# Kernel tuning notes

Measured on AMD Instinct MI355X. Metric: run time of the kernel, lower is better.

## Reference

```python
import jax, jax.numpy as jnp
import numpy as np

NUM_NODES = 512
HEADS = 4
IN_F = 256
OUT_F = 128
EPS = 1e-5


def _layernorm(x, g, b):
    mu = jnp.mean(x, axis=-1, keepdims=True)
    var = jnp.mean(jnp.square(x - mu), axis=-1, keepdims=True)
    return (x - mu) * jax.lax.rsqrt(var + EPS) * g + b


def setup_inputs() -> dict:
    key = jax.random.key(0)
    ks = jax.random.split(key, 16)
    N = 32 * NUM_NODES
    E = 262144
    s = 0.05
    return {
        "x": jax.random.normal(ks[0], (N, IN_F), jnp.float32),
        "edge_index": jax.random.randint(ks[1], (2, E), 0, N, jnp.int64),
        "W_l": jax.random.normal(ks[2], (IN_F, HEADS * OUT_F), jnp.float32) * s,
        "W_r": jax.random.normal(ks[3], (IN_F, HEADS * OUT_F), jnp.float32) * s,
        "att": jax.random.normal(ks[4], (HEADS, OUT_F), jnp.float32) * s,
        "gat_bias": jnp.zeros((OUT_F,), jnp.float32),
        "gat_gamma": jnp.ones((OUT_F,), jnp.float32),
        "gat_beta": jnp.zeros((OUT_F,), jnp.float32),
        "cnn_W": jax.random.normal(ks[5], (IN_F, OUT_F), jnp.float32) * s,
        "cnn_b": jnp.zeros((OUT_F,), jnp.float32),
        "conv_W": jax.random.normal(ks[6], (OUT_F, OUT_F, 7), jnp.float32) * s,
        "conv_b": jnp.zeros((OUT_F,), jnp.float32),
        "cnn_gamma": jnp.ones((OUT_F,), jnp.float32),
        "cnn_beta": jnp.zeros((OUT_F,), jnp.float32),
        "res_W": jax.random.normal(ks[7], (IN_F, OUT_F), jnp.float32) * s,
        "res_b": jnp.zeros((OUT_F,), jnp.float32),
        "fuse_gamma": jnp.ones((OUT_F,), jnp.float32),
        "fuse_beta": jnp.zeros((OUT_F,), jnp.float32),
    }


def reference(x, edge_index, W_l, W_r, att, gat_bias, gat_gamma, gat_beta,
              cnn_W, cnn_b, conv_W, conv_b, cnn_gamma, cnn_beta,
              res_W, res_b, fuse_gamma, fuse_beta):
    N = x.shape[0]
    B = N // NUM_NODES
    # --- GATv2 branch (add self-loops like PyG default) ---
    loop = jnp.arange(N, dtype=edge_index.dtype)
    src = jnp.concatenate([edge_index[0], loop])
    dst = jnp.concatenate([edge_index[1], loop])
    x_l = (x @ W_l).reshape(N, HEADS, OUT_F)
    x_r = (x @ W_r).reshape(N, HEADS, OUT_F)
    e = x_l[src] + x_r[dst]                      # [E+N, H, F]
    e = jnp.where(e > 0, e, 0.2 * e)             # leaky_relu, slope 0.2
    score = jnp.einsum('ehf,hf->eh', e, att)     # [E+N, H]
    m = jax.ops.segment_max(score, dst, num_segments=N)
    ex = jnp.exp(score - m[dst])
    denom = jax.ops.segment_sum(ex, dst, num_segments=N)
    alpha = ex / denom[dst]
    agg = jax.ops.segment_sum(alpha[:, :, None] * x_l[src], dst, num_segments=N)
    h_gat = jnp.mean(agg, axis=1) + gat_bias     # concat=False -> head mean
    h_gat = jnp.where(h_gat > 0, h_gat, 0.01 * h_gat)  # nn.LeakyReLU default
    h_gat = _layernorm(h_gat, gat_gamma, gat_beta)
    # --- CNN branch ---
    xc = x @ cnn_W + cnn_b                       # [N, F]
    xc = xc.reshape(B, NUM_NODES, OUT_F).transpose(0, 2, 1)  # [B, F, L]
    hc = jax.lax.conv_general_dilated(xc, conv_W, window_strides=(1,),
                                      padding=[(3, 3)],
                                      dimension_numbers=('NCW', 'OIW', 'NCW'))
    hc = hc + conv_b[None, :, None]
    hc = hc.transpose(0, 2, 1).reshape(N, OUT_F)
    hc = jax.nn.relu(hc)
    hc = _layernorm(hc, cnn_gamma, cnn_beta)
    # --- fuse + residual ---
    h = h_gat + hc + (x @ res_W + res_b)
    return _layernorm(h, fuse_gamma, fuse_beta)
```

## Files before the change

### kernel.cpp

```cpp
#include <hip/hip_runtime.h>
#include <hip/hip_bf16.h>
#include <math.h>

#define IN_F 256
#define OUT_F 128
#define HEADS 4
#define HF 512
#define NCAT 1280

typedef __hip_bfloat16 bf16;
typedef unsigned short ushort_t;
typedef unsigned char uchar_t;

using bf16x8 = __attribute__((ext_vector_type(8))) short;
using f32x4  = __attribute__((ext_vector_type(4))) float;

__device__ __forceinline__ float bflo(unsigned u) { return __uint_as_float(u << 16); }
__device__ __forceinline__ float bfhi(unsigned u) { return __uint_as_float(u & 0xffff0000u); }
__device__ __forceinline__ float bf2f(ushort_t u) { return __uint_as_float((unsigned)u << 16); }
__device__ __forceinline__ ushort_t f2bf(float f) {
    __hip_bfloat16 h = __float2bfloat16(f);
    return *reinterpret_cast<ushort_t*>(&h);
}

__device__ __forceinline__ void gload16(const void* g, void* l) {
    __builtin_amdgcn_global_load_lds(
        (const __attribute__((address_space(1))) unsigned int*)g,
        (__attribute__((address_space(3))) unsigned int*)l, 16, 0, 0);
}

template <int CTRL>
__device__ __forceinline__ float dpp_add(float s) {
    int t = __builtin_amdgcn_update_dpp(0, __float_as_int(s), CTRL, 0xf, 0xf, true);
    return s + __int_as_float(t);
}
__device__ __forceinline__ float rowsum16(float s) {
    s = dpp_add<0x121>(s);
    s = dpp_add<0x122>(s);
    s = dpp_add<0x124>(s);
    s = dpp_add<0x128>(s);
    return s;
}

__global__ __launch_bounds__(256) void prep_kernel(
    const float* __restrict__ x, ushort_t* __restrict__ xb, int n_cvt,
    const float* __restrict__ Wl, const float* __restrict__ Wr,
    const float* __restrict__ Wc, const float* __restrict__ Wres,
    const float* __restrict__ Wconv,
    ushort_t* __restrict__ Wt, ushort_t* __restrict__ Wt2,
    const int* __restrict__ ei, int* __restrict__ counts, int E,
    int g1, int g2) {
    int b = blockIdx.x;
    if (b < g1) {
        int i = (b * 256 + threadIdx.x) * 8;
        if (i >= n_cvt) return;
        float4 a = *(const float4*)(x + i);
        float4 c = *(const float4*)(x + i + 4);
        uint4 o;
        o.x = f2bf(a.x) | ((unsigned)f2bf(a.y) << 16);
        o.y = f2bf(a.z) | ((unsigned)f2bf(a.w) << 16);
        o.z = f2bf(c.x) | ((unsigned)f2bf(c.y) << 16);
        o.w = f2bf(c.z) | ((unsigned)f2bf(c.w) << 16);
        *(uint4*)(xb + i) = o;
    } else if (b < g2) {
        int idx = (b - g1) * 256 + threadIdx.x;
        if (idx < NCAT * 256) {
            int n = idx >> 8, k = idx & 255;
            float v;
            if (n < 512)       v = Wl[(size_t)k * 512 + n];
            else if (n < 1024) v = Wr[(size_t)k * 512 + (n - 512)];
            else if (n < 1152) v = Wc[(size_t)k * 128 + (n - 1024)];
            else               v = Wres[(size_t)k * 128 + (n - 1152)];
            Wt[idx] = f2bf(v);
        } else {
            int j = idx - NCAT * 256;
            if (j < 7 * 128 * 128) {
                int k = j >> 14, o = (j >> 7) & 127, i = j & 127;
                Wt2[j] = f2bf(Wconv[((size_t)o * 128 + i) * 7 + k]);
            }
        }
    } else {
        int e = (b - g2) * 256 + threadIdx.x;
        if (e < E) atomicAdd(&counts[ei[E + e]], 1);
    }
}

__global__ __launch_bounds__(256) void gemm_scatter_kernel(
    const ushort_t* __restrict__ A,
    const ushort_t* __restrict__ Wt,
    const float* __restrict__ att,
    uchar_t* __restrict__ xl8t, float2* __restrict__ saxl,
    ushort_t* __restrict__ xrb, ushort_t* __restrict__ xcb,
    ushort_t* __restrict__ resb,
    const int* __restrict__ ei, int* __restrict__ cursor,
    int* __restrict__ srcs, int E, int SB) {
    __shared__ __align__(1024) ushort_t As[128 * 64];
    __shared__ __align__(1024) ushort_t Bs[128 * 64];
    __shared__ float smax[128][2];
    __shared__ float paxl[128][2];
    if (blockIdx.x < SB) {
        int e = blockIdx.x * 256 + threadIdx.x;
        if (e < E) {
            int dd = ei[E + e];
            int pp = atomicAdd(&cursor[dd], 1);
            srcs[pp] = ei[e];
        }
        return;
    }
    int bid = blockIdx.x - SB;
    int by = bid / 10, bx = bid - by * 10;
    int tid = threadIdx.x;
    int lane = tid & 63, wid = tid >> 6;
    int wr = (wid >> 1) * 64, wc = (wid & 1) * 64;
    int brow = by * 128, bcol = bx * 128;
    int srow = lane >> 3;
    int sslot = lane & 7;
    int rl = lane & 15, kq = lane >> 4;
    f32x4 acc[4][4] = {};
    for (int k0 = 0; k0 < 256; k0 += 64) {
        #pragma unroll
        for (int j = 0; j < 4; ++j) {
            int r = (wid * 4 + j) * 8 + srow;
            int sl = sslot ^ (r & 7);
            gload16(A  + (size_t)(brow + r) * 256 + k0 + sl * 8,
                    (char*)As + (wid * 4 + j) * 1024);
            gload16(Wt + (size_t)(bcol + r) * 256 + k0 + sl * 8,
                    (char*)Bs + (wid * 4 + j) * 1024);
        }
        __syncthreads();
        #pragma unroll
        for (int ks = 0; ks < 2; ++ks) {
            int cb = ks * 64 + kq * 16;
            bf16x8 af[4], bfv[4];
            #pragma unroll
            for (int m = 0; m < 4; ++m) {
                int r = wr + m * 16 + rl;
                af[m] = *(const bf16x8*)((const char*)As + r * 128 + (cb ^ ((r & 7) << 4)));
            }
            #pragma unroll
            for (int n = 0; n < 4; ++n) {
                int r = wc + n * 16 + rl;
                bfv[n] = *(const bf16x8*)((const char*)Bs + r * 128 + (cb ^ ((r & 7) << 4)));
            }
            #pragma unroll
            for (int m = 0; m < 4; ++m)
                #pragma unroll
                for (int n = 0; n < 4; ++n)
                    acc[m][n] = __builtin_amdgcn_mfma_f32_16x16x32_bf16(
                        af[m], bfv[n], acc[m][n], 0, 0, 0);
        }
        __syncthreads();
    }
    int rowb = kq * 4;
    if (bcol < 512) {
        int head = bcol >> 7;
        float at[4];
        #pragma unroll
        for (int n = 0; n < 4; ++n) at[n] = att[bcol + wc + n * 16 + rl];
        #pragma unroll
        for (int m = 0; m < 4; ++m)
            #pragma unroll
            for (int q = 0; q < 4; ++q) {
                float t = fabsf(acc[m][0][q]);
                t = fmaxf(t, fabsf(acc[m][1][q]));
                t = fmaxf(t, fabsf(acc[m][2][q]));
                t = fmaxf(t, fabsf(acc[m][3][q]));
                #pragma unroll
                for (int o = 1; o < 16; o <<= 1) t = fmaxf(t, __shfl_xor(t, o));
                float p = 0.f;
                #pragma unroll
                for (int n = 0; n < 4; ++n) p = fmaf(at[n], acc[m][n][q], p);
                #pragma unroll
                for (int o = 1; o < 16; o <<= 1) p += __shfl_xor(p, o);
                if (rl == 0) {
                    int row = wr + m * 16 + rowb + q;
                    smax[row][wid & 1] = t;
                    paxl[row][wid & 1] = p;
                }
            }
        __syncthreads();
        #pragma unroll
        for (int m = 0; m < 4; ++m)
            #pragma unroll
            for (int q = 0; q < 4; ++q) {
                int row = wr + m * 16 + rowb + q;
                float sm = fmaxf(fmaxf(smax[row][0], smax[row][1]), 1e-8f);
                float s = sm * (1.f / 127.f);
                float rs = 127.f / sm;
                if ((wid & 1) == 0 && rl == 0) {
                    float axlf = 0.6f * 1.44269504f * (paxl[row][0] + paxl[row][1]);
                    saxl[(size_t)(brow + row) * 4 + head] = make_float2(s, axlf);
                }
                #pragma unroll
                for (int n = 0; n < 4; ++n) {
                    int col = bcol + wc + n * 16 + rl;
                    int qv = (int)rintf(acc[m][n][q] * rs) + 128;
                    xl8t[(size_t)(brow + row) * 512 + col] = (uchar_t)qv;
                }
            }
        return;
    }
    ushort_t* dstp; int cstride, cb2;
    if (bcol < 1024)      { dstp = xrb;  cstride = 512; cb2 = bcol - 512; }
    else if (bcol < 1152) { dstp = xcb;  cstride = 128; cb2 = bcol - 1024; }
    else                  { dstp = resb; cstride = 128; cb2 = bcol - 1152; }
    #pragma unroll
    for (int m = 0; m < 4; ++m)
        #pragma unroll
        for (int n = 0; n < 4; ++n) {
            int col = cb2 + wc + n * 16 + rl;
            #pragma unroll
            for (int q = 0; q < 4; ++q) {
                int row = brow + wr + m * 16 + rowb + q;
                dstp[(size_t)row * cstride + col] = f2bf(acc[m][n][q]);
            }
        }
}

__global__ __launch_bounds__(1024) void scan_kernel(
    const int* __restrict__ counts, int* __restrict__ offs,
    int* __restrict__ cursor, int N) {
    __shared__ int wsum[16];
    int t = threadIdx.x;
    int lane = t & 63, w = t >> 6;
    int base = t * 16;
    int local[16], s = 0;
    #pragma unroll
    for (int i = 0; i < 16; ++i) {
        int v = (base + i < N) ? counts[base + i] : 0;
        local[i] = v; s += v;
    }
    int sc = s;
    #pragma unroll
    for (int off = 1; off < 64; off <<= 1) {
        int v = __shfl_up(sc, off);
        if (lane >= off) sc += v;
    }
    if (lane == 63) wsum[w] = sc;
    __syncthreads();
    if (w == 0 && lane < 16) {
        int v = wsum[lane];
        int scv = v;
        #pragma unroll
        for (int off = 1; off < 16; off <<= 1) {
            int u = __shfl_up(scv, off);
            if (lane >= off) scv += u;
        }
        wsum[lane] = scv - v;
    }
    __syncthreads();
    int run = wsum[w] + sc - s;
    #pragma unroll
    for (int i = 0; i < 16; ++i) {
        if (base + i < N) { offs[base + i] = run; cursor[base + i] = run; }
        run += local[i];
    }
}

__global__ __launch_bounds__(256) void gat_kernel(
    const uchar_t* __restrict__ xl8t, const float2* __restrict__ saxl,
    const ushort_t* __restrict__ xrb,
    const int* __restrict__ srcs, const int* __restrict__ offs,
    const float* __restrict__ att, const float* __restrict__ gat_bias,
    const float* __restrict__ gat_gamma, const float* __restrict__ gat_beta,
    ushort_t* __restrict__ hgat_ln, int E, int N) {
    int wid = (blockIdx.x * 256 + threadIdx.x) >> 6;
    int lane = threadIdx.x & 63;
    if (wid >= N) return;
    int d = wid;
    int h = lane >> 4;
    const uint4 rv = ((const uint4*)(xrb + (size_t)d * HF))[lane];
    float xr8[8];
    xr8[0] = bflo(rv.x); xr8[1] = bfhi(rv.x);
    xr8[2] = bflo(rv.y); xr8[3] = bfhi(rv.y);
    xr8[4] = bflo(rv.z); xr8[5] = bfhi(rv.z);
    xr8[6] = bflo(rv.w); xr8[7] = bfhi(rv.w);
    const float LOG2E = 1.44269504f;
    const float4 a0 = ((const float4*)att)[lane * 2];
    const float4 a1 = ((const float4*)att)[lane * 2 + 1];
    const float aw[8] = {a0.x * LOG2E, a0.y * LOG2E, a0.z * LOG2E, a0.w * LOG2E,
                         a1.x * LOG2E, a1.y * LOG2E, a1.z * LOG2E, a1.w * LOG2E};
    float awm[8];
    #pragma unroll
    for (int j = 0; j < 8; ++j) awm[j] = 0.4f * aw[j];
    float axr_l = 0.f;
    #pragma unroll
    for (int j = 0; j < 8; ++j) axr_l = fmaf(aw[j], xr8[j], axr_l);
    float axrf = 0.6f * rowsum16(axr_l);

    float acc[8] = {};
    float dn = 0.f, sumexs = 0.f;

    auto process = [&](uint2 lv, float sc, float axlf) {
        float qf[8];
        qf[0] = (float)(lv.x & 0xff);         qf[1] = (float)((lv.x >> 8) & 0xff);
        qf[2] = (float)((lv.x >> 16) & 0xff); qf[3] = (float)(lv.x >> 24);
        qf[4] = (float)(lv.y & 0xff);         qf[5] = (float)((lv.y >> 8) & 0xff);
        qf[6] = (float)((lv.y >> 16) & 0xff); qf[7] = (float)(lv.y >> 24);
        float c = 128.f * sc;
        float s2a = 0.f, s2b = 0.f;
        #pragma unroll
        for (int j = 0; j < 4; ++j) {
            float v = fmaf(sc, qf[j], xr8[j]) - c;
            s2a = fmaf(fabsf(v), awm[j], s2a);
        }
        #pragma unroll
        for (int j = 4; j < 8; ++j) {
            float v = fmaf(sc, qf[j], xr8[j]) - c;
            s2b = fmaf(fabsf(v), awm[j], s2b);
        }
        float s = axlf + axrf + rowsum16(s2a + s2b);
        float ex = exp2f(s);
        float exs = ex * sc;
        dn += ex; sumexs += exs;
        #pragma unroll
        for (int j = 0; j < 8; ++j) acc[j] = fmaf(exs, qf[j], acc[j]);
    };

    {
        float2 sa = saxl[(size_t)d * 4 + h];
        process(((const uint2*)(xl8t + (size_t)d * 512))[lane], sa.x, sa.y);
    }

    int start = offs[d];
    int end = (d == N - 1) ? E : offs[d + 1];
    int nfull = (end - start) >> 2;
    int p = start;
    uint2 L0, L1, L2, L3;
    float2 S0, S1, S2, S3;
    if (nfull > 0) {
        int s0 = srcs[p], s1 = srcs[p + 1], s2 = srcs[p + 2], s3 = srcs[p + 3];
        L0 = ((const uint2*)(xl8t + (size_t)s0 * 512))[lane];
        L1 = ((const uint2*)(xl8t + (size_t)s1 * 512))[lane];
        L2 = ((const uint2*)(xl8t + (size_t)s2 * 512))[lane];
        L3 = ((const uint2*)(xl8t + (size_t)s3 * 512))[lane];
        S0 = saxl[(size_t)s0 * 4 + h];
        S1 = saxl[(size_t)s1 * 4 + h];
        S2 = saxl[(size_t)s2 * 4 + h];
        S3 = saxl[(size_t)s3 * 4 + h];
        p += 4;
    }
    for (int b = 1; b < nfull; ++b) {
        int s0 = srcs[p], s1 = srcs[p + 1], s2 = srcs[p + 2], s3 = srcs[p + 3];
        uint2 M0 = ((const uint2*)(xl8t + (size_t)s0 * 512))[lane];
        uint2 M1 = ((const uint2*)(xl8t + (size_t)s1 * 512))[lane];
        uint2 M2 = ((const uint2*)(xl8t + (size_t)s2 * 512))[lane];
        uint2 M3 = ((const uint2*)(xl8t + (size_t)s3 * 512))[lane];
        float2 T0 = saxl[(size_t)s0 * 4 + h];
        float2 T1 = saxl[(size_t)s1 * 4 + h];
        float2 T2 = saxl[(size_t)s2 * 4 + h];
        float2 T3 = saxl[(size_t)s3 * 4 + h];
        p += 4;
        process(L0, S0.x, S0.y); process(L1, S1.x, S1.y);
        process(L2, S2.x, S2.y); process(L3, S3.x, S3.y);
        L0 = M0; L1 = M1; L2 = M2; L3 = M3;
        S0 = T0; S1 = T1; S2 = T2; S3 = T3;
    }
    if (nfull > 0) {
        process(L0, S0.x, S0.y); process(L1, S1.x, S1.y);
        process(L2, S2.x, S2.y); process(L3, S3.x, S3.y);
    }
    for (; p < end; ++p) {
        int sp = srcs[p];
        float2 sa = saxl[(size_t)sp * 4 + h];
        process(((const uint2*)(xl8t + (size_t)sp * 512))[lane], sa.x, sa.y);
    }

    float inv = 1.f / dn;
    float corr = 128.f * sumexs;
    float v[8];
    #pragma unroll
    for (int j = 0; j < 8; ++j) {
        float t2 = (acc[j] - corr) * inv;
        t2 += __shfl_xor(t2, 16);
        t2 += __shfl_xor(t2, 32);
        v[j] = t2;
    }
    int col = (lane & 15) * 8 + 2 * h;
    float g0 = 0.25f * v[2 * h]     + gat_bias[col];
    float g1 = 0.25f * v[2 * h + 1] + gat_bias[col + 1];
    g0 = g0 > 0.f ? g0 : 0.01f * g0;
    g1 = g1 > 0.f ? g1 : 0.01f * g1;
    float s = g0 + g1;
    #pragma unroll
    for (int off = 32; off; off >>= 1) s += __shfl_xor(s, off);
    float mu = s * (1.f / 128.f);
    float d0 = g0 - mu, d1 = g1 - mu;
    float vs = d0 * d0 + d1 * d1;
    #pragma unroll
    for (int off = 32; off; off >>= 1) vs += __shfl_xor(vs, off);
    float rinv = rsqrtf(vs * (1.f / 128.f) + 1e-5f);
    float o0 = d0 * rinv * gat_gamma[col]     + gat_beta[col];
    float o1 = d1 * rinv * gat_gamma[col + 1] + gat_beta[col + 1];
    unsigned pk = (unsigned)f2bf(o0) | ((unsigned)f2bf(o1) << 16);
    *(unsigned*)(hgat_ln + (size_t)d * 128 + col) = pk;
}

__global__ __launch_bounds__(256) void conv_fuse_kernel(
    const ushort_t* __restrict__ xcb, const float* __restrict__ cnn_b,
    const ushort_t* __restrict__ Wt2, const float* __restrict__ conv_b,
    const float* __restrict__ cnn_gamma, const float* __restrict__ cnn_beta,
    const ushort_t* __restrict__ hgat_ln, const ushort_t* __restrict__ resb,
    const float* __restrict__ res_b,
    const float* __restrict__ fuse_gamma, const float* __restrict__ fuse_beta,
    float* __restrict__ out) {
    __shared__ ushort_t As[38][136];
    __shared__ __align__(1024) ushort_t Bs[128 * 128];
    __shared__ float hbuf[32][129];
    int tid = threadIdx.x;
    int lane = tid & 63, wid = tid >> 6;
    int wr = (wid >> 1) * 16, wc = (wid & 1) * 64;
    int b = blockIdx.y, l0 = blockIdx.x * 32;
    for (int u = tid; u < 38 * 16; u += 256) {
        int r = u >> 4, seg = u & 15;
        int l = l0 - 3 + r;
        uint4 o4 = make_uint4(0, 0, 0, 0);
        if (l >= 0 && l < 512) {
            uint4 v = *(const uint4*)(xcb + (size_t)(b * 512 + l) * 128 + seg * 8);
            float4 b0 = *(const float4*)(cnn_b + seg * 8);
            float4 b1 = *(const float4*)(cnn_b + seg * 8 + 4);
            o4.x = f2bf(bflo(v.x) + b0.x) | ((unsigned)f2bf(bfhi(v.x) + b0.y) << 16);
            o4.y = f2bf(bflo(v.y) + b0.z) | ((unsigned)f2bf(bfhi(v.y) + b0.w) << 16);
            o4.z = f2bf(bflo(v.z) + b1.x) | ((unsigned)f2bf(bfhi(v.z) + b1.y) << 16);
            o4.w = f2bf(bflo(v.w) + b1.z) | ((unsigned)f2bf(bfhi(v.w) + b1.w) << 16);
        }
        *(uint4*)&As[r][seg * 8] = o4;
    }
    f32x4 acc[4] = {};
    int rl = lane & 15, kb = (lane >> 4) * 8;
    int sr4 = lane >> 4, ss = lane & 15;
    for (int k = 0; k < 7; ++k) {
        __syncthreads();
        #pragma unroll
        for (int j = 0; j < 8; ++j) {
            int r = (wid * 8 + j) * 4 + sr4;
            int sl = ss ^ (r & 15);
            gload16(Wt2 + ((size_t)(k * 128 + r)) * 128 + sl * 8,
                    (char*)Bs + (wid * 8 + j) * 1024);
        }
        __syncthreads();
        #pragma unroll
        for (int kk = 0; kk < 4; ++kk) {
            bf16x8 af = *(const bf16x8*)&As[wr + rl + k][kk * 32 + kb];
            int cbyte = kk * 64 + (lane >> 4) * 16;
            #pragma unroll
            for (int n = 0; n < 4; ++n) {
                int r = wc + n * 16 + rl;
                bf16x8 bfr = *(const bf16x8*)((const char*)Bs + r * 256
                                              + (cbyte ^ ((r & 15) << 4)));
                acc[n] = __builtin_amdgcn_mfma_f32_16x16x32_bf16(af, bfr, acc[n], 0, 0, 0);
            }
        }
    }
    __syncthreads();
    int rowb = (lane >> 4) * 4;
    #pragma unroll
    for (int n = 0; n < 4; ++n) {
        int col = wc + n * 16 + rl;
        float cb = conv_b[col];
        #pragma unroll
        for (int q = 0; q < 4; ++q) {
            int r = wr + rowb + q;
            hbuf[r][col] = fmaxf(acc[n][q] + cb, 0.f);
        }
    }
    __syncthreads();
    for (int r = wid * 8; r < wid * 8 + 8; ++r) {
        int grow = b * 512 + l0 + r;
        float h0 = hbuf[r][lane], h1 = hbuf[r][lane + 64];
        float s = h0 + h1;
        #pragma unroll
        for (int off = 32; off; off >>= 1) s += __shfl_xor(s, off);
        float mu = s * (1.f / 128.f);
        float d0 = h0 - mu, d1 = h1 - mu;
        float vs = d0 * d0 + d1 * d1;
        #pragma unroll
        for (int off = 32; off; off >>= 1) vs += __shfl_xor(vs, off);
        float inv = rsqrtf(vs * (1.f / 128.f) + 1e-5f);
        float hcn0 = d0 * inv * cnn_gamma[lane]      + cnn_beta[lane];
        float hcn1 = d1 * inv * cnn_gamma[lane + 64] + cnn_beta[lane + 64];
        size_t base = (size_t)grow * 128;
        float v0 = bf2f(hgat_ln[base + lane])      + hcn0
                 + bf2f(resb[base + lane])      + res_b[lane];
        float v1 = bf2f(hgat_ln[base + lane + 64]) + hcn1
                 + bf2f(resb[base + lane + 64]) + res_b[lane + 64];
        s = v0 + v1;
        #pragma unroll
        for (int off = 32; off; off >>= 1) s += __shfl_xor(s, off);
        mu = s * (1.f / 128.f);
        d0 = v0 - mu; d1 = v1 - mu;
        vs = d0 * d0 + d1 * d1;
        #pragma unroll
        for (int off = 32; off; off >>= 1) vs += __shfl_xor(vs, off);
        inv = rsqrtf(vs * (1.f / 128.f) + 1e-5f);
        out[base + lane]      = d0 * inv * fuse_gamma[lane]      + fuse_beta[lane];
        out[base + lane + 64] = d1 * inv * fuse_gamma[lane + 64] + fuse_beta[lane + 64];
    }
}

extern "C" void kernel_launch(void* const* d_in, const int* in_sizes, int n_in,
                              void* d_out, int out_size, void* d_ws, size_t ws_size,
                              hipStream_t stream) {
    const float* x         = (const float*)d_in[0];
    const int*   ei        = (const int*)d_in[1];
    const float* W_l       = (const float*)d_in[2];
    const float* W_r       = (const float*)d_in[3];
    const float* att       = (const float*)d_in[4];
    const float* gat_bias  = (const float*)d_in[5];
    const float* gat_gamma = (const float*)d_in[6];
    const float* gat_beta  = (const float*)d_in[7];
    const float* cnn_W     = (const float*)d_in[8];
    const float* cnn_b     = (const float*)d_in[9];
    const float* conv_W    = (const float*)d_in[10];
    const float* conv_b    = (const float*)d_in[11];
    const float* cnn_gamma = (const float*)d_in[12];
    const float* cnn_beta  = (const float*)d_in[13];
    const float* res_W     = (const float*)d_in[14];
    const float* res_b     = (const float*)d_in[15];
    const float* fuse_gamma= (const float*)d_in[16];
    const float* fuse_beta = (const float*)d_in[17];

    int N = in_sizes[0] / IN_F;
    int E = in_sizes[1] / 2;

    char* ws = (char*)d_ws;
    size_t off = 0;
    ushort_t* xb     = (ushort_t*)(ws + off); off += (size_t)N * IN_F * 2;
    ushort_t* Wt     = (ushort_t*)(ws + off); off += (size_t)NCAT * IN_F * 2;
    ushort_t* Wt2    = (ushort_t*)(ws + off); off += (size_t)7 * 128 * 128 * 2;
    uchar_t*  xl8t   = (uchar_t*)(ws + off);  off += (size_t)N * HF;
    float2*   saxl   = (float2*)(ws + off);   off += (size_t)N * 4 * 8;
    ushort_t* xrb    = (ushort_t*)(ws + off); off += (size_t)N * HF * 2;
    ushort_t* xcb    = (ushort_t*)(ws + off); off += (size_t)N * 128 * 2;
    ushort_t* resb   = (ushort_t*)(ws + off); off += (size_t)N * 128 * 2;
    ushort_t* hgat_ln= (ushort_t*)(ws + off); off += (size_t)N * 128 * 2;
    int*  counts     = (int*)(ws + off);  off += (size_t)N * 4;
    int*  offs       = (int*)(ws + off);  off += (size_t)N * 4;
    int*  cursor     = (int*)(ws + off);  off += (size_t)N * 4;
    int*  srcs       = (int*)(ws + off);  off += (size_t)E * 4;

    hipMemsetAsync(counts, 0, (size_t)N * 4, stream);

    dim3 blk(256);
    int n_cvt = N * IN_F;
    int g1 = (n_cvt / 8 + 255) / 256;
    int g2 = g1 + (NCAT * 256 + 7 * 128 * 128 + 255) / 256;
    int g3 = g2 + (E + 255) / 256;
    prep_kernel<<<g3, blk, 0, stream>>>(x, xb, n_cvt,
        W_l, W_r, cnn_W, res_W, conv_W, Wt, Wt2, ei, counts, E, g1, g2);

    scan_kernel<<<1, 1024, 0, stream>>>(counts, offs, cursor, N);

    int SB = (E + 255) / 256;
    gemm_scatter_kernel<<<SB + (NCAT / 128) * (N / 128), blk, 0, stream>>>(
        xb, Wt, att, xl8t, saxl, xrb, xcb, resb, ei, cursor, srcs, E, SB);

    gat_kernel<<<(N + 3) / 4, blk, 0, stream>>>(
        xl8t, saxl, xrb, srcs, offs, att, gat_bias, gat_gamma, gat_beta,
        hgat_ln, E, N);

    conv_fuse_kernel<<<dim3(16, 32), blk, 0, stream>>>(
        xcb, cnn_b, Wt2, conv_b, cnn_gamma, cnn_beta,
        hgat_ln, resb, res_b, fuse_gamma, fuse_beta, (float*)d_out);
}
```

Baseline: 153.5 us.

## Reorder conv before GAT and fuse final layernorm into GAT kernel

The conv kernel now runs first and writes its CNN-branch layernorm output as bf16. The GAT kernel then reads that output plus the residual and does the final fuse and layernorm in its epilogue, writing float2 outputs. The fused residual and layernorm work moves off the conv kernel and rides on the memory-bound GAT wave, and the GAT-side intermediate buffer round-trip goes away. The per-edge score math is also simplified to a single 8-term accumulation with the 0.4 factor applied after the row sum, which may shift float rounding slightly.

```diff
diff --git a/kernel.cpp b/kernel.cpp
--- a/kernel.cpp
+++ b/kernel.cpp
@@ -257,153 +257,11 @@
     }
 }
 
-__global__ __launch_bounds__(256) void gat_kernel(
-    const uchar_t* __restrict__ xl8t, const float2* __restrict__ saxl,
-    const ushort_t* __restrict__ xrb,
-    const int* __restrict__ srcs, const int* __restrict__ offs,
-    const float* __restrict__ att, const float* __restrict__ gat_bias,
-    const float* __restrict__ gat_gamma, const float* __restrict__ gat_beta,
-    ushort_t* __restrict__ hgat_ln, int E, int N) {
-    int wid = (blockIdx.x * 256 + threadIdx.x) >> 6;
-    int lane = threadIdx.x & 63;
-    if (wid >= N) return;
-    int d = wid;
-    int h = lane >> 4;
-    const uint4 rv = ((const uint4*)(xrb + (size_t)d * HF))[lane];
-    float xr8[8];
-    xr8[0] = bflo(rv.x); xr8[1] = bfhi(rv.x);
-    xr8[2] = bflo(rv.y); xr8[3] = bfhi(rv.y);
-    xr8[4] = bflo(rv.z); xr8[5] = bfhi(rv.z);
-    xr8[6] = bflo(rv.w); xr8[7] = bfhi(rv.w);
-    const float LOG2E = 1.44269504f;
-    const float4 a0 = ((const float4*)att)[lane * 2];
-    const float4 a1 = ((const float4*)att)[lane * 2 + 1];
-    const float aw[8] = {a0.x * LOG2E, a0.y * LOG2E, a0.z * LOG2E, a0.w * LOG2E,
-                         a1.x * LOG2E, a1.y * LOG2E, a1.z * LOG2E, a1.w * LOG2E};
-    float awm[8];
-    #pragma unroll
-    for (int j = 0; j < 8; ++j) awm[j] = 0.4f * aw[j];
-    float axr_l = 0.f;
-    #pragma unroll
-    for (int j = 0; j < 8; ++j) axr_l = fmaf(aw[j], xr8[j], axr_l);
-    float axrf = 0.6f * rowsum16(axr_l);
-
-    float acc[8] = {};
-    float dn = 0.f, sumexs = 0.f;
-
-    auto process = [&](uint2 lv, float sc, float axlf) {
-        float qf[8];
-        qf[0] = (float)(lv.x & 0xff);         qf[1] = (float)((lv.x >> 8) & 0xff);
-        qf[2] = (float)((lv.x >> 16) & 0xff); qf[3] = (float)(lv.x >> 24);
-        qf[4] = (float)(lv.y & 0xff);         qf[5] = (float)((lv.y >> 8) & 0xff);
-        qf[6] = (float)((lv.y >> 16) & 0xff); qf[7] = (float)(lv.y >> 24);
-        float c = 128.f * sc;
-        float s2a = 0.f, s2b = 0.f;
-        #pragma unroll
-        for (int j = 0; j < 4; ++j) {
-            float v = fmaf(sc, qf[j], xr8[j]) - c;
-            s2a = fmaf(fabsf(v), awm[j], s2a);
-        }
-        #pragma unroll
-        for (int j = 4; j < 8; ++j) {
-            float v = fmaf(sc, qf[j], xr8[j]) - c;
-            s2b = fmaf(fabsf(v), awm[j], s2b);
-        }
-        float s = axlf + axrf + rowsum16(s2a + s2b);
-        float ex = exp2f(s);
-        float exs = ex * sc;
-        dn += ex; sumexs += exs;
-        #pragma unroll
-        for (int j = 0; j < 8; ++j) acc[j] = fmaf(exs, qf[j], acc[j]);
-    };
-
-    {
-        float2 sa = saxl[(size_t)d * 4 + h];
-        process(((const uint2*)(xl8t + (size_t)d * 512))[lane], sa.x, sa.y);
-    }
-
-    int start = offs[d];
-    int end = (d == N - 1) ? E : offs[d + 1];
-    int nfull = (end - start) >> 2;
-    int p = start;
-    uint2 L0, L1, L2, L3;
-    float2 S0, S1, S2, S3;
-    if (nfull > 0) {
-        int s0 = srcs[p], s1 = srcs[p + 1], s2 = srcs[p + 2], s3 = srcs[p + 3];
-        L0 = ((const uint2*)(xl8t + (size_t)s0 * 512))[lane];
-        L1 = ((const uint2*)(xl8t + (size_t)s1 * 512))[lane];
-        L2 = ((const uint2*)(xl8t + (size_t)s2 * 512))[lane];
-        L3 = ((const uint2*)(xl8t + (size_t)s3 * 512))[lane];
-        S0 = saxl[(size_t)s0 * 4 + h];
-        S1 = saxl[(size_t)s1 * 4 + h];
-        S2 = saxl[(size_t)s2 * 4 + h];
-        S3 = saxl[(size_t)s3 * 4 + h];
-        p += 4;
-    }
-    for (int b = 1; b < nfull; ++b) {
-        int s0 = srcs[p], s1 = srcs[p + 1], s2 = srcs[p + 2], s3 = srcs[p + 3];
-        uint2 M0 = ((const uint2*)(xl8t + (size_t)s0 * 512))[lane];
-        uint2 M1 = ((const uint2*)(xl8t + (size_t)s1 * 512))[lane];
-        uint2 M2 = ((const uint2*)(xl8t + (size_t)s2 * 512))[lane];
-        uint2 M3 = ((const uint2*)(xl8t + (size_t)s3 * 512))[lane];
-        float2 T0 = saxl[(size_t)s0 * 4 + h];
-        float2 T1 = saxl[(size_t)s1 * 4 + h];
-        float2 T2 = saxl[(size_t)s2 * 4 + h];
-        float2 T3 = saxl[(size_t)s3 * 4 + h];
-        p += 4;
-        process(L0, S0.x, S0.y); process(L1, S1.x, S1.y);
-        process(L2, S2.x, S2.y); process(L3, S3.x, S3.y);
-        L0 = M0; L1 = M1; L2 = M2; L3 = M3;
-        S0 = T0; S1 = T1; S2 = T2; S3 = T3;
-    }
-    if (nfull > 0) {
-        process(L0, S0.x, S0.y); process(L1, S1.x, S1.y);
-        process(L2, S2.x, S2.y); process(L3, S3.x, S3.y);
-    }
-    for (; p < end; ++p) {
-        int sp = srcs[p];
-        float2 sa = saxl[(size_t)sp * 4 + h];
-        process(((const uint2*)(xl8t + (size_t)sp * 512))[lane], sa.x, sa.y);
-    }
-
-    float inv = 1.f / dn;
-    float corr = 128.f * sumexs;
-    float v[8];
-    #pragma unroll
-    for (int j = 0; j < 8; ++j) {
-        float t2 = (acc[j] - corr) * inv;
-        t2 += __shfl_xor(t2, 16);
-        t2 += __shfl_xor(t2, 32);
-        v[j] = t2;
-    }
-    int col = (lane & 15) * 8 + 2 * h;
-    float g0 = 0.25f * v[2 * h]     + gat_bias[col];
-    float g1 = 0.25f * v[2 * h + 1] + gat_bias[col + 1];
-    g0 = g0 > 0.f ? g0 : 0.01f * g0;
-    g1 = g1 > 0.f ? g1 : 0.01f * g1;
-    float s = g0 + g1;
-    #pragma unroll
-    for (int off = 32; off; off >>= 1) s += __shfl_xor(s, off);
-    float mu = s * (1.f / 128.f);
-    float d0 = g0 - mu, d1 = g1 - mu;
-    float vs = d0 * d0 + d1 * d1;
-    #pragma unroll
-    for (int off = 32; off; off >>= 1) vs += __shfl_xor(vs, off);
-    float rinv = rsqrtf(vs * (1.f / 128.f) + 1e-5f);
-    float o0 = d0 * rinv * gat_gamma[col]     + gat_beta[col];
-    float o1 = d1 * rinv * gat_gamma[col + 1] + gat_beta[col + 1];
-    unsigned pk = (unsigned)f2bf(o0) | ((unsigned)f2bf(o1) << 16);
-    *(unsigned*)(hgat_ln + (size_t)d * 128 + col) = pk;
-}
-
-__global__ __launch_bounds__(256) void conv_fuse_kernel(
+__global__ __launch_bounds__(256) void conv_ln_kernel(
     const ushort_t* __restrict__ xcb, const float* __restrict__ cnn_b,
     const ushort_t* __restrict__ Wt2, const float* __restrict__ conv_b,
     const float* __restrict__ cnn_gamma, const float* __restrict__ cnn_beta,
-    const ushort_t* __restrict__ hgat_ln, const ushort_t* __restrict__ resb,
-    const float* __restrict__ res_b,
-    const float* __restrict__ fuse_gamma, const float* __restrict__ fuse_beta,
-    float* __restrict__ out) {
+    ushort_t* __restrict__ hcn_ln) {
     __shared__ ushort_t As[38][136];
     __shared__ __align__(1024) ushort_t Bs[128 * 128];
     __shared__ float hbuf[32][129];
@@ -477,25 +335,159 @@
         #pragma unroll
         for (int off = 32; off; off >>= 1) vs += __shfl_xor(vs, off);
         float inv = rsqrtf(vs * (1.f / 128.f) + 1e-5f);
-        float hcn0 = d0 * inv * cnn_gamma[lane]      + cnn_beta[lane];
-        float hcn1 = d1 * inv * cnn_gamma[lane + 64] + cnn_beta[lane + 64];
         size_t base = (size_t)grow * 128;
-        float v0 = bf2f(hgat_ln[base + lane])      + hcn0
-                 + bf2f(resb[base + lane])      + res_b[lane];
-        float v1 = bf2f(hgat_ln[base + lane + 64]) + hcn1
-                 + bf2f(resb[base + lane + 64]) + res_b[lane + 64];
-        s = v0 + v1;
-        #pragma unroll
-        for (int off = 32; off; off >>= 1) s += __shfl_xor(s, off);
-        mu = s * (1.f / 128.f);
-        d0 = v0 - mu; d1 = v1 - mu;
-        vs = d0 * d0 + d1 * d1;
-        #pragma unroll
-        for (int off = 32; off; off >>= 1) vs += __shfl_xor(vs, off);
-        inv = rsqrtf(vs * (1.f / 128.f) + 1e-5f);
-        out[base + lane]      = d0 * inv * fuse_gamma[lane]      + fuse_beta[lane];
-        out[base + lane + 64] = d1 * inv * fuse_gamma[lane + 64] + fuse_beta[lane + 64];
-    }
+        hcn_ln[base + lane]      = f2bf(d0 * inv * cnn_gamma[lane]      + cnn_beta[lane]);
+        hcn_ln[base + lane + 64] = f2bf(d1 * inv * cnn_gamma[lane + 64] + cnn_beta[lane + 64]);
+    }
+}
+
+__global__ __launch_bounds__(256) void gat_final_kernel(
+    const uchar_t* __restrict__ xl8t, const float2* __restrict__ saxl,
+    const ushort_t* __restrict__ xrb,
+    const int* __restrict__ srcs, const int* __restrict__ offs,
+    const float* __restrict__ att, const float* __restrict__ gat_bias,
+    const float* __restrict__ gat_gamma, const float* __restrict__ gat_beta,
+    const ushort_t* __restrict__ hcn_ln, const ushort_t* __restrict__ resb,
+    const float* __restrict__ res_b,
+    const float* __restrict__ fuse_gamma, const float* __restrict__ fuse_beta,
+    float* __restrict__ out, int E, int N) {
+    int wid = (blockIdx.x * 256 + threadIdx.x) >> 6;
+    int lane = threadIdx.x & 63;
+    if (wid >= N) return;
+    int d = wid;
+    int h = lane >> 4;
+    const uint4 rv = ((const uint4*)(xrb + (size_t)d * HF))[lane];
+    float xr8[8];
+    xr8[0] = bflo(rv.x); xr8[1] = bfhi(rv.x);
+    xr8[2] = bflo(rv.y); xr8[3] = bfhi(rv.y);
+    xr8[4] = bflo(rv.z); xr8[5] = bfhi(rv.z);
+    xr8[6] = bflo(rv.w); xr8[7] = bfhi(rv.w);
+    const float LOG2E = 1.44269504f;
+    const float4 a0 = ((const float4*)att)[lane * 2];
+    const float4 a1 = ((const float4*)att)[lane * 2 + 1];
+    const float aw[8] = {a0.x * LOG2E, a0.y * LOG2E, a0.z * LOG2E, a0.w * LOG2E,
+                         a1.x * LOG2E, a1.y * LOG2E, a1.z * LOG2E, a1.w * LOG2E};
+    float axr_l = 0.f;
+    #pragma unroll
+    for (int j = 0; j < 8; ++j) axr_l = fmaf(aw[j], xr8[j], axr_l);
+    float axrf = 0.6f * rowsum16(axr_l);
+
+    float acc[8] = {};
+    float dn = 0.f, sumexs = 0.f;
+
+    auto process = [&](uint2 lv, float sc, float axlf) {
+        float qf[8];
+        qf[0] = (float)(lv.x & 0xff);         qf[1] = (float)((lv.x >> 8) & 0xff);
+        qf[2] = (float)((lv.x >> 16) & 0xff); qf[3] = (float)(lv.x >> 24);
+        qf[4] = (float)(lv.y & 0xff);         qf[5] = (float)((lv.y >> 8) & 0xff);
+        qf[6] = (float)((lv.y >> 16) & 0xff); qf[7] = (float)(lv.y >> 24);
+        float c = 128.f * sc;
+        float s2 = 0.f;
+        #pragma unroll
+        for (int j = 0; j < 8; ++j) {
+            float v = fmaf(sc, qf[j], xr8[j]) - c;
+            s2 = fmaf(fabsf(v), aw[j], s2);
+        }
+        float s = fmaf(0.4f, rowsum16(s2), axlf + axrf);
+        float ex = exp2f(s);
+        float exs = ex * sc;
+        dn += ex; sumexs += exs;
+        #pragma unroll
+        for (int j = 0; j < 8; ++j) acc[j] = fmaf(exs, qf[j], acc[j]);
+    };
+
+    {
+        float2 sa = saxl[(size_t)d * 4 + h];
+        process(((const uint2*)(xl8t + (size_t)d * 512))[lane], sa.x, sa.y);
+    }
+
+    int start = offs[d];
+    int end = (d == N - 1) ? E : offs[d + 1];
+    int nfull = (end - start) >> 2;
+    int p = start;
+    uint2 L0, L1, L2, L3;
+    float2 S0, S1, S2, S3;
+    if (nfull > 0) {
+        int s0 = srcs[p], s1 = srcs[p + 1], s2 = srcs[p + 2], s3 = srcs[p + 3];
+        L0 = ((const uint2*)(xl8t + (size_t)s0 * 512))[lane];
+        L1 = ((const uint2*)(xl8t + (size_t)s1 * 512))[lane];
+        L2 = ((const uint2*)(xl8t + (size_t)s2 * 512))[lane];
+        L3 = ((const uint2*)(xl8t + (size_t)s3 * 512))[lane];
+        S0 = saxl[(size_t)s0 * 4 + h];
+        S1 = saxl[(size_t)s1 * 4 + h];
+        S2 = saxl[(size_t)s2 * 4 + h];
+        S3 = saxl[(size_t)s3 * 4 + h];
+        p += 4;
+    }
+    for (int b = 1; b < nfull; ++b) {
+        int s0 = srcs[p], s1 = srcs[p + 1], s2 = srcs[p + 2], s3 = srcs[p + 3];
+        uint2 M0 = ((const uint2*)(xl8t + (size_t)s0 * 512))[lane];
+        uint2 M1 = ((const uint2*)(xl8t + (size_t)s1 * 512))[lane];
+        uint2 M2 = ((const uint2*)(xl8t + (size_t)s2 * 512))[lane];
+        uint2 M3 = ((const uint2*)(xl8t + (size_t)s3 * 512))[lane];
+        float2 T0 = saxl[(size_t)s0 * 4 + h];
+        float2 T1 = saxl[(size_t)s1 * 4 + h];
+        float2 T2 = saxl[(size_t)s2 * 4 + h];
+        float2 T3 = saxl[(size_t)s3 * 4 + h];
+        p += 4;
+        process(L0, S0.x, S0.y); process(L1, S1.x, S1.y);
+        process(L2, S2.x, S2.y); process(L3, S3.x, S3.y);
+        L0 = M0; L1 = M1; L2 = M2; L3 = M3;
+        S0 = T0; S1 = T1; S2 = T2; S3 = T3;
+    }
+    if (nfull > 0) {
+        process(L0, S0.x, S0.y); process(L1, S1.x, S1.y);
+        process(L2, S2.x, S2.y); process(L3, S3.x, S3.y);
+    }
+    for (; p < end; ++p) {
+        int sp = srcs[p];
+        float2 sa = saxl[(size_t)sp * 4 + h];
+        process(((const uint2*)(xl8t + (size_t)sp * 512))[lane], sa.x, sa.y);
+    }
+
+    float inv = 1.f / dn;
+    float corr = 128.f * sumexs;
+    float v[8];
+    #pragma unroll
+    for (int j = 0; j < 8; ++j) {
+        float t2 = (acc[j] - corr) * inv;
+        t2 += __shfl_xor(t2, 16);
+        t2 += __shfl_xor(t2, 32);
+        v[j] = t2;
+    }
+    int col = (lane & 15) * 8 + 2 * h;
+    float g0 = 0.25f * v[2 * h]     + gat_bias[col];
+    float g1 = 0.25f * v[2 * h + 1] + gat_bias[col + 1];
+    g0 = g0 > 0.f ? g0 : 0.01f * g0;
+    g1 = g1 > 0.f ? g1 : 0.01f * g1;
+    float s = g0 + g1;
+    #pragma unroll
+    for (int off = 32; off; off >>= 1) s += __shfl_xor(s, off);
+    float mu = s * (1.f / 128.f);
+    float d0 = g0 - mu, d1 = g1 - mu;
+    float vs = d0 * d0 + d1 * d1;
+    #pragma unroll
+    for (int off = 32; off; off >>= 1) vs += __shfl_xor(vs, off);
+    float rinv = rsqrtf(vs * (1.f / 128.f) + 1e-5f);
+    float hg0 = d0 * rinv * gat_gamma[col]     + gat_beta[col];
+    float hg1 = d1 * rinv * gat_gamma[col + 1] + gat_beta[col + 1];
+    size_t base = (size_t)d * 128 + col;
+    unsigned hcu = *(const unsigned*)(hcn_ln + base);
+    unsigned rsu = *(const unsigned*)(resb + base);
+    float v0 = hg0 + bflo(hcu) + bflo(rsu) + res_b[col];
+    float v1 = hg1 + bfhi(hcu) + bfhi(rsu) + res_b[col + 1];
+    s = v0 + v1;
+    #pragma unroll
+    for (int off = 32; off; off >>= 1) s += __shfl_xor(s, off);
+    mu = s * (1.f / 128.f);
+    d0 = v0 - mu; d1 = v1 - mu;
+    vs = d0 * d0 + d1 * d1;
+    #pragma unroll
+    for (int off = 32; off; off >>= 1) vs += __shfl_xor(vs, off);
+    rinv = rsqrtf(vs * (1.f / 128.f) + 1e-5f);
+    float2 o2 = make_float2(d0 * rinv * fuse_gamma[col]     + fuse_beta[col],
+                            d1 * rinv * fuse_gamma[col + 1] + fuse_beta[col + 1]);
+    *(float2*)(out + base) = o2;
 }
 
 extern "C" void kernel_launch(void* const* d_in, const int* in_sizes, int n_in,
@@ -533,7 +525,7 @@
     ushort_t* xrb    = (ushort_t*)(ws + off); off += (size_t)N * HF * 2;
     ushort_t* xcb    = (ushort_t*)(ws + off); off += (size_t)N * 128 * 2;
     ushort_t* resb   = (ushort_t*)(ws + off); off += (size_t)N * 128 * 2;
-    ushort_t* hgat_ln= (ushort_t*)(ws + off); off += (size_t)N * 128 * 2;
+    ushort_t* hcn_ln = (ushort_t*)(ws + off); off += (size_t)N * 128 * 2;
     int*  counts     = (int*)(ws + off);  off += (size_t)N * 4;
     int*  offs       = (int*)(ws + off);  off += (size_t)N * 4;
     int*  cursor     = (int*)(ws + off);  off += (size_t)N * 4;
@@ -555,11 +547,10 @@
     gemm_scatter_kernel<<<SB + (NCAT / 128) * (N / 128), blk, 0, stream>>>(
         xb, Wt, att, xl8t, saxl, xrb, xcb, resb, ei, cursor, srcs, E, SB);
 
-    gat_kernel<<<(N + 3) / 4, blk, 0, stream>>>(
+    conv_ln_kernel<<<dim3(16, 32), blk, 0, stream>>>(
+        xcb, cnn_b, Wt2, conv_b, cnn_gamma, cnn_beta, hcn_ln);
+
+    gat_final_kernel<<<(N + 3) / 4, blk, 0, stream>>>(
         xl8t, saxl, xrb, srcs, offs, att, gat_bias, gat_gamma, gat_beta,
-        hgat_ln, E, N);
-
-    conv_fuse_kernel<<<dim3(16, 32), blk, 0, stream>>>(
-        xcb, cnn_b, Wt2, conv_b, cnn_gamma, cnn_beta,
-        hgat_ln, resb, res_b, fuse_gamma, fuse_beta, (float*)d_out);
-}
+        hcn_ln, resb, res_b, fuse_gamma, fuse_beta, (float*)d_out, E, N);
+}
```

Result: faster. 140.2 us (-8.7%).
